# Optimization experiments

Hardware: AMD Instinct MI355X
Metric: run time of the kernel (lower is better)

The kernel has to match this reference:

```python
import jax, jax.numpy as jnp
import numpy as np

D = 512      # emb_size
H = 8        # attention heads
E = 8        # num experts
HID = 512    # expert MLP hidden (assumed StandardExpert = 2-layer MLP)
NTOK = 8192  # 8*1024 tokens
W_IMP = 0.01


def setup_inputs() -> dict:
    key = jax.random.key(0)
    ks = jax.random.split(key, 16)
    f = lambda i, shape, s=0.02: (jax.random.normal(ks[i], shape, jnp.float32) * s)
    return {
        "x": jax.random.normal(ks[0], (8, 1024, D), jnp.float32),
        "q": jax.random.normal(ks[1], (NTOK, D), jnp.float32),
        "Wq": f(2, (D, D)), "bq": jnp.zeros((D,), jnp.float32),
        "Wk": f(3, (D, D)), "bk": jnp.zeros((D,), jnp.float32),
        "Wv": f(4, (D, D)), "bv": jnp.zeros((D,), jnp.float32),
        "Wo": f(5, (D, D)), "bo": jnp.zeros((D,), jnp.float32),
        "gate_W": f(6, (D, E)), "gate_b": jnp.zeros((E,), jnp.float32),
        "W1": f(7, (E, D, HID)), "b1": jnp.zeros((E, HID), jnp.float32),
        "W2": f(8, (E, HID, D)), "b2": jnp.zeros((E, D), jnp.float32),
        "top": 2,
    }


def _cross_att(xf, q, Wq, bq, Wk, bk, Wv, bv, Wo, bo):
    # seq_len == 1 on both sides after unsqueeze(1) in the torch code
    N, d = xf.shape
    dh = d // H
    Q = (xf @ Wq + bq).reshape(N, H, dh)
    K = (q @ Wk + bk).reshape(N, H, dh)
    V = (q @ Wv + bv).reshape(N, H, dh)
    scores = jnp.sum(Q * K, axis=-1, keepdims=True) / jnp.sqrt(jnp.float32(dh))  # [N,H,1]
    w = jax.nn.softmax(scores, axis=-1)  # trivially ones (single key), kept for fidelity
    att = (w * V).reshape(N, d)
    return att @ Wo + bo


def reference(x, q, Wq, bq, Wk, bk, Wv, bv, Wo, bo, gate_W, gate_b, W1, b1, W2, b2, top):
    x_shape = x.shape
    xf = x.reshape(-1, x_shape[-1])  # [N, D]
    att = _cross_att(xf, q, Wq, bq, Wk, bk, Wv, bv, Wo, bo)
    gate_logits = att @ gate_W + gate_b
    gate_prob = jax.nn.softmax(gate_logits, axis=-1)  # [N, E] (eval mode: no noise)
    top_w, top_i = jax.lax.top_k(gate_prob, top)       # [N, top]
    top_w = jax.nn.softmax(top_w, axis=-1)
    # combine weights per expert: comb[n,e] = sum_k top_w[n,k] * [top_i[n,k]==e]
    comb = jnp.sum(top_w[..., None] * jax.nn.one_hot(top_i, E, dtype=xf.dtype), axis=1)  # [N, E]
    y = jnp.zeros_like(xf)
    for e in range(E):  # fixed small expert loop; dense compute + mask-combine
        h = jax.nn.relu(xf @ W1[e] + b1[e])
        ye = h @ W2[e] + b2[e]
        y = y + comb[:, e:e + 1] * ye
    importance = gate_prob.sum(axis=0)  # [E]
    # torch.std uses ddof=1
    importance_loss = W_IMP * (jnp.std(importance, ddof=1) / jnp.mean(importance)) ** 2
    return y.reshape(x_shape), gate_prob, importance_loss
```

## Files before the change

### kernel.cpp

```cpp
#include <hip/hip_runtime.h>
#include <math.h>
#include <stdint.h>

#define NTOK 8192
#define DIM  512
#define NEXP 8
#define HIDN 512
#define BM 64
#define BN 128
#define BK 32
#define NT  (DIM / BK)
#define MAXRB 136
#define SLOTS (MAXRB*BM)
#define GBLK (NTOK/16)

typedef _Float16 f16;
typedef __attribute__((ext_vector_type(4))) _Float16 f16x4;
typedef __attribute__((ext_vector_type(8))) _Float16 f16x8;
typedef __attribute__((ext_vector_type(4))) float    f32x4;

__device__ __forceinline__ void gl2lds16(const void* g, void* l) {
  __builtin_amdgcn_global_load_lds(
      (const __attribute__((address_space(1))) unsigned int*)(g),
      (__attribute__((address_space(3))) unsigned int*)(l), 16, 0, 0);
}

__global__ __launch_bounds__(256) void k_prep(
    const float* __restrict__ x, f16* __restrict__ xh,
    const float* __restrict__ W1, const float* __restrict__ W2,
    f16* __restrict__ W1t, f16* __restrict__ W2t,
    const float* __restrict__ Wo, const float* __restrict__ gW,
    double* __restrict__ G1) {
  const int bx = blockIdx.x, tid = threadIdx.x;
  if (bx < 4096) {
    int i4 = (bx * 256 + tid) * 4;
    float4 v = *(const float4*)(x + i4);
    f16x4 o; o.x = (_Float16)v.x; o.y = (_Float16)v.y; o.z = (_Float16)v.z; o.w = (_Float16)v.w;
    *(f16x4*)(xh + i4) = o;
  } else if (bx < 8192) {
    __shared__ float t[32][33];
    int idx = bx - 4096;
    int z = idx >> 8, rem = idx & 255;
    int k0 = (rem >> 4) * 32, n0 = (rem & 15) * 32;
    const float* src = (z < 8 ? W1 : W2) + (size_t)(z & 7) * DIM * DIM;
    f16* dst = (z < 8 ? W1t : W2t) + (size_t)(z & 7) * DIM * DIM;
    int tx = tid & 31, ty = tid >> 5;
    for (int r = ty; r < 32; r += 8) t[r][tx] = src[(size_t)(k0 + r) * DIM + n0 + tx];
    __syncthreads();
    for (int r = ty; r < 32; r += 8) dst[(size_t)(n0 + r) * DIM + k0 + tx] = (f16)t[tx][r];
  } else {
    int out = (bx - 8192) * 4 + (tid >> 6);
    int lane = tid & 63;
    int d = out >> 3, e = out & 7;
    double acc = 0.0;
#pragma unroll
    for (int j = 0; j < 8; j++) {
      int k = j * 64 + lane;
      acc += (double)Wo[d * DIM + k] * (double)gW[k * NEXP + e];
    }
#pragma unroll
    for (int off = 32; off; off >>= 1) acc += __shfl_xor(acc, off, 64);
    if (lane == 0) G1[out] = acc;
  }
}

__global__ void k_foldB(const float* __restrict__ Wv, const double* __restrict__ G1,
                        float* __restrict__ Wg, const float* __restrict__ bv,
                        const float* __restrict__ bo, const float* __restrict__ gW,
                        const float* __restrict__ gb, double* __restrict__ bg) {
  int lane = threadIdx.x & 63;
  if (blockIdx.x == 1024) {
    int w = threadIdx.x >> 6;
    for (int e = w; e < NEXP; e += 4) {
      double acc = 0.0;
#pragma unroll
      for (int j = 0; j < 8; j++) {
        int d = j * 64 + lane;
        acc += (double)bv[d] * G1[d * NEXP + e] + (double)bo[d] * (double)gW[d * NEXP + e];
      }
#pragma unroll
      for (int off = 32; off; off >>= 1) acc += __shfl_xor(acc, off, 64);
      if (lane == 0) bg[e] = acc + (double)gb[e];
    }
    return;
  }
  int out = blockIdx.x * 4 + (threadIdx.x >> 6);
  int d = out >> 3, e = out & 7;
  double acc = 0.0;
#pragma unroll
  for (int j = 0; j < 8; j++) {
    int k = j * 64 + lane;
    acc += (double)Wv[d * DIM + k] * G1[k * NEXP + e];
  }
#pragma unroll
  for (int off = 32; off; off >>= 1) acc += __shfl_xor(acc, off, 64);
  if (lane == 0) Wg[out] = (float)acc;
}

__global__ __launch_bounds__(256) void k_gate(
    const float* __restrict__ q, const float* __restrict__ Wg,
    const double* __restrict__ bg, float* __restrict__ gp_out,
    int* __restrict__ e1a, int* __restrict__ e2a,
    float* __restrict__ w1a, float* __restrict__ w2a,
    int* __restrict__ r1a, int* __restrict__ r2a, int* __restrict__ hist,
    float* __restrict__ gpsum) {
  __shared__ float qs[16 * 513];
  __shared__ float ps[16][8];
  __shared__ int cnt[16];
  const int tid = threadIdx.x;
  const int tok0 = blockIdx.x * 16;

  for (int i = tid; i < 16 * 512; i += 256) {
    int r = i >> 9, c = i & 511;
    qs[r * 513 + c] = q[(size_t)(tok0 + r) * DIM + c];
  }
  if (tid < 16) cnt[tid] = 0;
  __syncthreads();

  const int e = tid & 7;
  const int half = (tid >> 3) & 1;
  const int tl = tid >> 4;
  const float* qrow = qs + tl * 513 + half * 256;
  const float* wcol = Wg + half * 256 * NEXP + e;

  double a0 = 0, a1 = 0, a2 = 0, a3 = 0;
#pragma unroll 4
  for (int j = 0; j < 256; j += 4) {
    a0 += (double)qrow[j]     * (double)wcol[(size_t)j * NEXP];
    a1 += (double)qrow[j + 1] * (double)wcol[(size_t)(j + 1) * NEXP];
    a2 += (double)qrow[j + 2] * (double)wcol[(size_t)(j + 2) * NEXP];
    a3 += (double)qrow[j + 3] * (double)wcol[(size_t)(j + 3) * NEXP];
  }
  double acc = (a0 + a1) + (a2 + a3);
  acc += __shfl_xor(acc, 8, 64);

  double l = acc + bg[e];
  double m = l;
#pragma unroll
  for (int off = 1; off < 8; off <<= 1) m = fmax(m, __shfl_xor(m, off, 64));
  float ex = expf((float)(l - m));
  float s = ex;
#pragma unroll
  for (int off = 1; off < 8; off <<= 1) s += __shfl_xor(s, off, 64);
  float pf = ex / s;
  int tok = tok0 + tl;
  if (half == 0) { gp_out[(size_t)tok * NEXP + e] = pf; ps[tl][e] = pf; }

  double v1 = l; int i1 = e;
#pragma unroll
  for (int off = 1; off < 8; off <<= 1) {
    double ov = __shfl_xor(v1, off, 64);
    int oi = __shfl_xor(i1, off, 64);
    if (ov > v1 || (ov == v1 && oi < i1)) { v1 = ov; i1 = oi; }
  }
  double v2 = (e == i1) ? -1e300 : l; int i2 = e;
#pragma unroll
  for (int off = 1; off < 8; off <<= 1) {
    double ov = __shfl_xor(v2, off, 64);
    int oi = __shfl_xor(i2, off, 64);
    if (ov > v2 || (ov == v2 && oi < i2)) { v2 = ov; i2 = oi; }
  }
  float p1 = __shfl(pf, (tl << 4) + i1, 64);
  float p2 = __shfl(pf, (tl << 4) + i2, 64);
  if (e == 0 && half == 0) {
    float ev = expf(p2 - p1);
    float iw = 1.0f / (1.0f + ev);
    e1a[tok] = i1; e2a[tok] = i2;
    w1a[tok] = iw; w2a[tok] = ev * iw;
    r1a[tok] = atomicAdd(&cnt[i1], 1);
    r2a[tok] = atomicAdd(&cnt[8 + i2], 1);
  }
  __syncthreads();
  if (tid < 16) hist[blockIdx.x * 16 + tid] = cnt[tid];
  if (tid < 8) {
    float ssum = 0.f;
#pragma unroll
    for (int r = 0; r < 16; r++) ssum += ps[r][tid];
    gpsum[blockIdx.x * 8 + tid] = ssum;
  }
}

__global__ __launch_bounds__(1024) void k_route(
    const int* __restrict__ hist,
    const int* __restrict__ e1a, const int* __restrict__ e2a,
    const float* __restrict__ w1a, const float* __restrict__ w2a,
    const int* __restrict__ r1a, const int* __restrict__ r2a,
    int* __restrict__ aoff, int* __restrict__ counts,
    int* __restrict__ toks, float* __restrict__ wsl,
    const float* __restrict__ gpsum, float* __restrict__ loss) {
  __shared__ int bb[GBLK][16];
  __shared__ int tot[16];
  __shared__ int s_ao[16];
  __shared__ double imp[8];
  const int c = threadIdx.x >> 6;
  const int l = threadIdx.x & 63;
  int v[GBLK / 64];
  int s = 0;
#pragma unroll
  for (int j = 0; j < GBLK / 64; j++) {
    v[j] = hist[((l * (GBLK / 64) + j) << 4) + c];
    s += v[j];
  }
  int incl = s;
#pragma unroll
  for (int off = 1; off < 64; off <<= 1) {
    int t = __shfl_up(incl, off, 64);
    if (l >= off) incl += t;
  }
  int run = incl - s;
#pragma unroll
  for (int j = 0; j < GBLK / 64; j++) {
    bb[l * (GBLK / 64) + j][c] = run;
    run += v[j];
  }
  if (l == 63) tot[c] = incl;
  __syncthreads();
  if (threadIdx.x == 0) {
    int o0 = 0, o1 = 0;
#pragma unroll
    for (int e = 0; e < NEXP; e++) {
      s_ao[e] = o0;     o0 += (tot[e] + BM - 1) / BM * BM;
      s_ao[8 + e] = o1; o1 += (tot[8 + e] + BM - 1) / BM * BM;
    }
    if (blockIdx.x == 0) {
      int p0 = 0, p1 = 0;
#pragma unroll
      for (int e = 0; e < NEXP; e++) {
        counts[e] = tot[e];         aoff[e] = p0;     p0 += (tot[e] + BM - 1) / BM * BM;
        counts[8 + e] = tot[8 + e]; aoff[9 + e] = p1; p1 += (tot[8 + e] + BM - 1) / BM * BM;
      }
      aoff[8] = p0; aoff[17] = p1;
    }
  }
  __syncthreads();
  if (blockIdx.x == 0) {
    const int cnt_c = tot[c];
    const int padded = (cnt_c + BM - 1) / BM * BM;
    const int base = ((c >> 3) ? SLOTS : 0) + s_ao[c];
    for (int sidx = cnt_c + l; sidx < padded; sidx += 64)
      toks[base + sidx] = 0;
    if (c < 8) {
      double a = 0.0;
#pragma unroll
      for (int j = 0; j < GBLK / 64; j++)
        a += (double)gpsum[(size_t)(l + j * 64) * 8 + c];
#pragma unroll
      for (int off = 32; off; off >>= 1) a += __shfl_xor(a, off, 64);
      if (l == 0) imp[c] = a;
    }
    __syncthreads();
    if (threadIdx.x == 0) {
      double mn = 0.0;
      for (int e = 0; e < 8; e++) mn += imp[e];
      mn *= (1.0 / 8.0);
      double var = 0.0;
      for (int e = 0; e < 8; e++) { double d = imp[e] - mn; var += d * d; }
      var *= (1.0 / 7.0);
      double r = sqrt(var) / mn;
      loss[0] = (float)(0.01 * r * r);
    }
  }
  if (threadIdx.x < 256) {
    int n = blockIdx.x * 256 + threadIdx.x;
    int blk = n >> 4;
    int e1 = e1a[n];
    int slot = s_ao[e1] + bb[blk][e1] + r1a[n];
    toks[slot] = n; wsl[slot] = w1a[n];
    int e2 = e2a[n];
    slot = SLOTS + s_ao[8 + e2] + bb[blk][8 + e2] + r2a[n];
    toks[slot] = n; wsl[slot] = w2a[n];
  }
}

template <int MODE>
__global__ __launch_bounds__(256) void k_expert(
    const f16* __restrict__ Asrc, const f16* __restrict__ Wt,
    const float* __restrict__ bias, const int* __restrict__ toks,
    const float* __restrict__ wsl, const int* __restrict__ aoff,
    const int* __restrict__ counts, f16* __restrict__ Hout,
    float* __restrict__ y, float* __restrict__ ypart) {
  const int klist = blockIdx.z;
  const int* ao = aoff + klist * 9;
  const int slot0 = blockIdx.x * BM;
  if (slot0 >= ao[8]) return;
  int e = 0;
#pragma unroll
  for (int t = 1; t <= 7; t++) if (slot0 >= ao[t]) e = t;

  const int n0 = blockIdx.y * BN;
  const int tid = threadIdx.x, lane = tid & 63, wid = tid >> 6;

  __shared__ __align__(16) f16 As[2][BM * BK];
  __shared__ __align__(16) f16 Bs[2][BN * BK];

  const int srow = wid * 16 + (lane >> 2);
  const int scol = (lane & 3) * 8;

  const f16* arow;
  if (MODE == 0) {
    int tk = toks[klist * SLOTS + slot0 + srow];
    arow = Asrc + (size_t)tk * DIM + scol;
  } else {
    arow = Asrc + (size_t)(klist * SLOTS + slot0 + srow) * HIDN + scol;
  }
  const f16* brow[2];
  int bloff[2];
#pragma unroll
  for (int rnd = 0; rnd < 2; rnd++) {
    brow[rnd] = Wt + ((size_t)e * DIM + n0 + rnd * 64 + srow) * DIM + scol;
    bloff[rnd] = (rnd * 64 + wid * 16) * BK;
  }
  const int aloff = wid * 16 * BK;

  f32x4 acc[4][2] = {};
  const int fr = lane & 15, kb = (lane >> 4) * 8;

#define STAGE(buf, ks)                                    \
  {                                                       \
    gl2lds16(arow + (ks), As[buf] + aloff);               \
    _Pragma("unroll")                                     \
    for (int rnd = 0; rnd < 2; rnd++)                     \
      gl2lds16(brow[rnd] + (ks), Bs[buf] + bloff[rnd]);   \
  }

  STAGE(0, 0);
  __syncthreads();
  for (int t = 0; t < NT; t++) {
    const int cur = t & 1;
    if (t + 1 < NT) STAGE(cur ^ 1, (t + 1) * BK);
    f16x8 af[4], bf[2];
#pragma unroll
    for (int m = 0; m < 4; m++)
      af[m] = *(const f16x8*)(As[cur] + (m * 16 + fr) * BK + kb);
#pragma unroll
    for (int n = 0; n < 2; n++)
      bf[n] = *(const f16x8*)(Bs[cur] + (wid * 32 + n * 16 + fr) * BK + kb);
#pragma unroll
    for (int m = 0; m < 4; m++)
#pragma unroll
      for (int n = 0; n < 2; n++)
        acc[m][n] = __builtin_amdgcn_mfma_f32_16x16x32_f16(af[m], bf[n], acc[m][n], 0, 0, 0);
    __syncthreads();
  }
#undef STAGE

  float bcol[2];
#pragma unroll
  for (int n = 0; n < 2; n++)
    bcol[n] = bias[e * ((MODE == 0) ? HIDN : DIM) + n0 + wid * 32 + n * 16 + fr];

  if (MODE == 0) {
#pragma unroll
    for (int m = 0; m < 4; m++)
#pragma unroll
      for (int r4 = 0; r4 < 4; r4++) {
        int slot = slot0 + m * 16 + (lane >> 4) * 4 + r4;
#pragma unroll
        for (int n = 0; n < 2; n++) {
          int col = n0 + wid * 32 + n * 16 + fr;
          float v = acc[m][n][r4] + bcol[n];
          Hout[(size_t)(klist * SLOTS + slot) * HIDN + col] = (f16)fmaxf(v, 0.f);
        }
      }
  } else {
    float* yo = (klist == 0) ? y : ypart;
    const int vend = ao[e] + counts[klist * 8 + e];
#pragma unroll
    for (int m = 0; m < 4; m++)
#pragma unroll
      for (int r4 = 0; r4 < 4; r4++) {
        int slot = slot0 + m * 16 + (lane >> 4) * 4 + r4;
        if (slot < vend) {
          int tk = toks[klist * SLOTS + slot];
          float w = wsl[klist * SLOTS + slot];
#pragma unroll
          for (int n = 0; n < 2; n++) {
            int col = n0 + wid * 32 + n * 16 + fr;
            yo[(size_t)tk * DIM + col] = (acc[m][n][r4] + bcol[n]) * w;
          }
        }
      }
  }
}

__global__ __launch_bounds__(256) void k_combine(float* __restrict__ y,
                                                 const float* __restrict__ ypart) {
  size_t i4 = ((size_t)blockIdx.x * 256 + threadIdx.x) * 4;
  float4 a = *(const float4*)(y + i4);
  float4 b = *(const float4*)(ypart + i4);
  a.x += b.x; a.y += b.y; a.z += b.z; a.w += b.w;
  *(float4*)(y + i4) = a;
}

extern "C" void kernel_launch(void* const* d_in, const int* in_sizes, int n_in,
                              void* d_out, int out_size, void* d_ws, size_t ws_size,
                              hipStream_t stream) {
  const float* x  = (const float*)d_in[0];
  const float* q  = (const float*)d_in[1];
  const float* Wv = (const float*)d_in[6];
  const float* bv = (const float*)d_in[7];
  const float* Wo = (const float*)d_in[8];
  const float* bo = (const float*)d_in[9];
  const float* gW = (const float*)d_in[10];
  const float* gb = (const float*)d_in[11];
  const float* W1 = (const float*)d_in[12];
  const float* b1 = (const float*)d_in[13];
  const float* W2 = (const float*)d_in[14];
  const float* b2 = (const float*)d_in[15];

  float* out = (float*)d_out;
  float* y_out = out;
  float* gp_out = out + (size_t)NTOK * DIM;
  float* loss_out = gp_out + (size_t)NTOK * NEXP;

  uint8_t* w = (uint8_t*)d_ws;
  size_t o = 0;
  auto alloc = [&](size_t bytes) -> void* {
    void* p = w + o;
    o = (o + bytes + 255) & ~(size_t)255;
    return p;
  };
  f16* xh      = (f16*)alloc((size_t)NTOK * DIM * 2);
  f16* W1t     = (f16*)alloc((size_t)NEXP * DIM * HIDN * 2);
  f16* W2t     = (f16*)alloc((size_t)NEXP * DIM * HIDN * 2);
  f16* Hbuf    = (f16*)alloc((size_t)2 * SLOTS * HIDN * 2);
  float* ypart = (float*)alloc((size_t)NTOK * DIM * 4);
  double* G1   = (double*)alloc((size_t)DIM * NEXP * 8);
  float* Wg    = (float*)alloc((size_t)DIM * NEXP * 4);
  double* bg   = (double*)alloc(NEXP * 8);
  int* e1a     = (int*)alloc(NTOK * 4);
  int* e2a     = (int*)alloc(NTOK * 4);
  float* w1a   = (float*)alloc(NTOK * 4);
  float* w2a   = (float*)alloc(NTOK * 4);
  int* r1a     = (int*)alloc(NTOK * 4);
  int* r2a     = (int*)alloc(NTOK * 4);
  int* hist    = (int*)alloc((size_t)GBLK * 16 * 4);
  float* gpsum = (float*)alloc((size_t)GBLK * 8 * 4);
  int* counts  = (int*)alloc(16 * 4);
  int* aoff    = (int*)alloc(18 * 4);
  int* toks    = (int*)alloc((size_t)2 * SLOTS * 4);
  float* wsl   = (float*)alloc((size_t)2 * SLOTS * 4);
  (void)ws_size; (void)in_sizes; (void)n_in; (void)out_size;

  k_prep<<<9216, 256, 0, stream>>>(x, xh, W1, W2, W1t, W2t, Wo, gW, G1);
  k_foldB<<<1025, 256, 0, stream>>>(Wv, G1, Wg, bv, bo, gW, gb, bg);
  k_gate<<<GBLK, 256, 0, stream>>>(q, Wg, bg, gp_out, e1a, e2a, w1a, w2a, r1a, r2a, hist, gpsum);
  k_route<<<NTOK / 256, 1024, 0, stream>>>(hist, e1a, e2a, w1a, w2a, r1a, r2a,
                                           aoff, counts, toks, wsl, gpsum, loss_out);
  k_expert<0><<<dim3(MAXRB, 4, 2), 256, 0, stream>>>(xh, W1t, b1, toks, wsl, aoff, counts,
                                                     Hbuf, nullptr, nullptr);
  k_expert<1><<<dim3(MAXRB, 4, 2), 256, 0, stream>>>(Hbuf, W2t, b2, toks, wsl, aoff, counts,
                                                     nullptr, y_out, ypart);
  k_combine<<<NTOK * DIM / 1024, 256, 0, stream>>>(y_out, ypart);
}
```

Baseline: 103.0 us.

## Fuse prep, fold, gate and route into one cooperative kernel with grid syncs

Replaces four front-end launches (prep, foldB, gate, route) with a single cooperative kernel of 512 blocks that walks each phase in a grid-stride loop and separates phases with grid.sync(). The goal is to remove launch gaps and tail idle time between small dependent kernels. The routing prefix sum is now recomputed redundantly per block from the global histogram, and the work-bearing phases run on fewer resident blocks. Grid barriers add their own latency and cap parallelism at the 512 co-resident blocks.

```diff
diff --git a/kernel.cpp b/kernel.cpp
--- a/kernel.cpp
+++ b/kernel.cpp
@@ -1,6 +1,9 @@
 #include <hip/hip_runtime.h>
+#include <hip/hip_cooperative_groups.h>
 #include <math.h>
 #include <stdint.h>
+
+namespace cg = cooperative_groups;
 
 #define NTOK 8192
 #define DIM  512
@@ -13,6 +16,7 @@
 #define MAXRB 136
 #define SLOTS (MAXRB*BM)
 #define GBLK (NTOK/16)
+#define FBLK 512
 
 typedef _Float16 f16;
 typedef __attribute__((ext_vector_type(4))) _Float16 f16x4;
@@ -25,250 +29,252 @@
       (__attribute__((address_space(3))) unsigned int*)(l), 16, 0, 0);
 }
 
-__global__ __launch_bounds__(256) void k_prep(
-    const float* __restrict__ x, f16* __restrict__ xh,
-    const float* __restrict__ W1, const float* __restrict__ W2,
-    f16* __restrict__ W1t, f16* __restrict__ W2t,
-    const float* __restrict__ Wo, const float* __restrict__ gW,
-    double* __restrict__ G1) {
-  const int bx = blockIdx.x, tid = threadIdx.x;
-  if (bx < 4096) {
-    int i4 = (bx * 256 + tid) * 4;
-    float4 v = *(const float4*)(x + i4);
-    f16x4 o; o.x = (_Float16)v.x; o.y = (_Float16)v.y; o.z = (_Float16)v.z; o.w = (_Float16)v.w;
-    *(f16x4*)(xh + i4) = o;
-  } else if (bx < 8192) {
-    __shared__ float t[32][33];
-    int idx = bx - 4096;
-    int z = idx >> 8, rem = idx & 255;
-    int k0 = (rem >> 4) * 32, n0 = (rem & 15) * 32;
-    const float* src = (z < 8 ? W1 : W2) + (size_t)(z & 7) * DIM * DIM;
-    f16* dst = (z < 8 ? W1t : W2t) + (size_t)(z & 7) * DIM * DIM;
-    int tx = tid & 31, ty = tid >> 5;
-    for (int r = ty; r < 32; r += 8) t[r][tx] = src[(size_t)(k0 + r) * DIM + n0 + tx];
-    __syncthreads();
-    for (int r = ty; r < 32; r += 8) dst[(size_t)(n0 + r) * DIM + k0 + tx] = (f16)t[tx][r];
-  } else {
-    int out = (bx - 8192) * 4 + (tid >> 6);
+struct FrontArgs {
+  const float* x;  f16* xh;
+  const float* W1; const float* W2; f16* W1t; f16* W2t;
+  const float* Wo; const float* gW; double* G1;
+  const float* Wv; const float* bv; const float* bo; const float* gb;
+  float* Wg; double* bg;
+  const float* q;  float* gp_out;
+  int* e1a; int* e2a; float* w1a; float* w2a; int* r1a; int* r2a;
+  int* hist; float* gpsum;
+  int* aoff; int* counts; int* toks; float* wsl; float* loss;
+};
+
+union SMem {
+  struct { float qs[16 * 513]; float ps[16][8]; int cnt[16]; } g;
+  struct { float t[32][33]; } tr;
+  struct {
+    int sfull[16][16]; int sbelow[16][16];
+    int tot[16]; int pre[16]; int s_ao[16];
+    double simp[32][8]; double imp[8];
+  } r;
+};
+
+__global__ __launch_bounds__(256) void k_front(FrontArgs a) {
+  cg::grid_group grid = cg::this_grid();
+  __shared__ SMem sm;
+  const int tid = threadIdx.x;
+  const int b = blockIdx.x;
+
+  for (int u = b; u < 9216; u += FBLK) {
+    if (u < 4096) {
+      int i4 = (u * 256 + tid) * 4;
+      float4 v = *(const float4*)(a.x + i4);
+      f16x4 o; o.x = (_Float16)v.x; o.y = (_Float16)v.y; o.z = (_Float16)v.z; o.w = (_Float16)v.w;
+      *(f16x4*)(a.xh + i4) = o;
+    } else if (u < 8192) {
+      int idx = u - 4096;
+      int z = idx >> 8, rem = idx & 255;
+      int k0 = (rem >> 4) * 32, n0 = (rem & 15) * 32;
+      const float* src = (z < 8 ? a.W1 : a.W2) + (size_t)(z & 7) * DIM * DIM;
+      f16* dst = (z < 8 ? a.W1t : a.W2t) + (size_t)(z & 7) * DIM * DIM;
+      int tx = tid & 31, ty = tid >> 5;
+      __syncthreads();
+      for (int r = ty; r < 32; r += 8) sm.tr.t[r][tx] = src[(size_t)(k0 + r) * DIM + n0 + tx];
+      __syncthreads();
+      for (int r = ty; r < 32; r += 8) dst[(size_t)(n0 + r) * DIM + k0 + tx] = (f16)sm.tr.t[tx][r];
+      __syncthreads();
+    } else {
+      int out = (u - 8192) * 4 + (tid >> 6);
+      int lane = tid & 63;
+      int d = out >> 3, e = out & 7;
+      double acc = 0.0;
+#pragma unroll
+      for (int j = 0; j < 8; j++) {
+        int k = j * 64 + lane;
+        acc += (double)a.Wo[d * DIM + k] * (double)a.gW[k * NEXP + e];
+      }
+#pragma unroll
+      for (int off = 32; off; off >>= 1) acc += __shfl_xor(acc, off, 64);
+      if (lane == 0) a.G1[out] = acc;
+    }
+  }
+  grid.sync();
+
+  for (int u = b; u < 1025; u += FBLK) {
     int lane = tid & 63;
-    int d = out >> 3, e = out & 7;
-    double acc = 0.0;
-#pragma unroll
-    for (int j = 0; j < 8; j++) {
-      int k = j * 64 + lane;
-      acc += (double)Wo[d * DIM + k] * (double)gW[k * NEXP + e];
-    }
-#pragma unroll
-    for (int off = 32; off; off >>= 1) acc += __shfl_xor(acc, off, 64);
-    if (lane == 0) G1[out] = acc;
-  }
-}
-
-__global__ void k_foldB(const float* __restrict__ Wv, const double* __restrict__ G1,
-                        float* __restrict__ Wg, const float* __restrict__ bv,
-                        const float* __restrict__ bo, const float* __restrict__ gW,
-                        const float* __restrict__ gb, double* __restrict__ bg) {
-  int lane = threadIdx.x & 63;
-  if (blockIdx.x == 1024) {
-    int w = threadIdx.x >> 6;
-    for (int e = w; e < NEXP; e += 4) {
+    if (u == 1024) {
+      int w = tid >> 6;
+      for (int e = w; e < NEXP; e += 4) {
+        double acc = 0.0;
+#pragma unroll
+        for (int j = 0; j < 8; j++) {
+          int d = j * 64 + lane;
+          acc += (double)a.bv[d] * a.G1[d * NEXP + e] + (double)a.bo[d] * (double)a.gW[d * NEXP + e];
+        }
+#pragma unroll
+        for (int off = 32; off; off >>= 1) acc += __shfl_xor(acc, off, 64);
+        if (lane == 0) a.bg[e] = acc + (double)a.gb[e];
+      }
+    } else {
+      int out = u * 4 + (tid >> 6);
+      int d = out >> 3, e = out & 7;
       double acc = 0.0;
 #pragma unroll
       for (int j = 0; j < 8; j++) {
-        int d = j * 64 + lane;
-        acc += (double)bv[d] * G1[d * NEXP + e] + (double)bo[d] * (double)gW[d * NEXP + e];
+        int k = j * 64 + lane;
+        acc += (double)a.Wv[d * DIM + k] * a.G1[k * NEXP + e];
       }
 #pragma unroll
       for (int off = 32; off; off >>= 1) acc += __shfl_xor(acc, off, 64);
-      if (lane == 0) bg[e] = acc + (double)gb[e];
-    }
-    return;
-  }
-  int out = blockIdx.x * 4 + (threadIdx.x >> 6);
-  int d = out >> 3, e = out & 7;
-  double acc = 0.0;
-#pragma unroll
-  for (int j = 0; j < 8; j++) {
-    int k = j * 64 + lane;
-    acc += (double)Wv[d * DIM + k] * G1[k * NEXP + e];
-  }
-#pragma unroll
-  for (int off = 32; off; off >>= 1) acc += __shfl_xor(acc, off, 64);
-  if (lane == 0) Wg[out] = (float)acc;
-}
-
-__global__ __launch_bounds__(256) void k_gate(
-    const float* __restrict__ q, const float* __restrict__ Wg,
-    const double* __restrict__ bg, float* __restrict__ gp_out,
-    int* __restrict__ e1a, int* __restrict__ e2a,
-    float* __restrict__ w1a, float* __restrict__ w2a,
-    int* __restrict__ r1a, int* __restrict__ r2a, int* __restrict__ hist,
-    float* __restrict__ gpsum) {
-  __shared__ float qs[16 * 513];
-  __shared__ float ps[16][8];
-  __shared__ int cnt[16];
-  const int tid = threadIdx.x;
-  const int tok0 = blockIdx.x * 16;
-
-  for (int i = tid; i < 16 * 512; i += 256) {
-    int r = i >> 9, c = i & 511;
-    qs[r * 513 + c] = q[(size_t)(tok0 + r) * DIM + c];
-  }
-  if (tid < 16) cnt[tid] = 0;
-  __syncthreads();
-
-  const int e = tid & 7;
-  const int half = (tid >> 3) & 1;
-  const int tl = tid >> 4;
-  const float* qrow = qs + tl * 513 + half * 256;
-  const float* wcol = Wg + half * 256 * NEXP + e;
-
-  double a0 = 0, a1 = 0, a2 = 0, a3 = 0;
+      if (lane == 0) a.Wg[out] = (float)acc;
+    }
+  }
+  grid.sync();
+
+  {
+    const int tok0 = b * 16;
+    __syncthreads();
+    for (int i = tid; i < 16 * 512; i += 256) {
+      int r = i >> 9, c = i & 511;
+      sm.g.qs[r * 513 + c] = a.q[(size_t)(tok0 + r) * DIM + c];
+    }
+    if (tid < 16) sm.g.cnt[tid] = 0;
+    __syncthreads();
+
+    const int e = tid & 7;
+    const int half = (tid >> 3) & 1;
+    const int tl = tid >> 4;
+    const float* qrow = sm.g.qs + tl * 513 + half * 256;
+    const float* wcol = a.Wg + half * 256 * NEXP + e;
+
+    double a0 = 0, a1 = 0, a2 = 0, a3 = 0;
 #pragma unroll 4
-  for (int j = 0; j < 256; j += 4) {
-    a0 += (double)qrow[j]     * (double)wcol[(size_t)j * NEXP];
-    a1 += (double)qrow[j + 1] * (double)wcol[(size_t)(j + 1) * NEXP];
-    a2 += (double)qrow[j + 2] * (double)wcol[(size_t)(j + 2) * NEXP];
-    a3 += (double)qrow[j + 3] * (double)wcol[(size_t)(j + 3) * NEXP];
-  }
-  double acc = (a0 + a1) + (a2 + a3);
-  acc += __shfl_xor(acc, 8, 64);
-
-  double l = acc + bg[e];
-  double m = l;
-#pragma unroll
-  for (int off = 1; off < 8; off <<= 1) m = fmax(m, __shfl_xor(m, off, 64));
-  float ex = expf((float)(l - m));
-  float s = ex;
-#pragma unroll
-  for (int off = 1; off < 8; off <<= 1) s += __shfl_xor(s, off, 64);
-  float pf = ex / s;
-  int tok = tok0 + tl;
-  if (half == 0) { gp_out[(size_t)tok * NEXP + e] = pf; ps[tl][e] = pf; }
-
-  double v1 = l; int i1 = e;
-#pragma unroll
-  for (int off = 1; off < 8; off <<= 1) {
-    double ov = __shfl_xor(v1, off, 64);
-    int oi = __shfl_xor(i1, off, 64);
-    if (ov > v1 || (ov == v1 && oi < i1)) { v1 = ov; i1 = oi; }
-  }
-  double v2 = (e == i1) ? -1e300 : l; int i2 = e;
-#pragma unroll
-  for (int off = 1; off < 8; off <<= 1) {
-    double ov = __shfl_xor(v2, off, 64);
-    int oi = __shfl_xor(i2, off, 64);
-    if (ov > v2 || (ov == v2 && oi < i2)) { v2 = ov; i2 = oi; }
-  }
-  float p1 = __shfl(pf, (tl << 4) + i1, 64);
-  float p2 = __shfl(pf, (tl << 4) + i2, 64);
-  if (e == 0 && half == 0) {
-    float ev = expf(p2 - p1);
-    float iw = 1.0f / (1.0f + ev);
-    e1a[tok] = i1; e2a[tok] = i2;
-    w1a[tok] = iw; w2a[tok] = ev * iw;
-    r1a[tok] = atomicAdd(&cnt[i1], 1);
-    r2a[tok] = atomicAdd(&cnt[8 + i2], 1);
-  }
-  __syncthreads();
-  if (tid < 16) hist[blockIdx.x * 16 + tid] = cnt[tid];
-  if (tid < 8) {
-    float ssum = 0.f;
-#pragma unroll
-    for (int r = 0; r < 16; r++) ssum += ps[r][tid];
-    gpsum[blockIdx.x * 8 + tid] = ssum;
-  }
-}
-
-__global__ __launch_bounds__(1024) void k_route(
-    const int* __restrict__ hist,
-    const int* __restrict__ e1a, const int* __restrict__ e2a,
-    const float* __restrict__ w1a, const float* __restrict__ w2a,
-    const int* __restrict__ r1a, const int* __restrict__ r2a,
-    int* __restrict__ aoff, int* __restrict__ counts,
-    int* __restrict__ toks, float* __restrict__ wsl,
-    const float* __restrict__ gpsum, float* __restrict__ loss) {
-  __shared__ int bb[GBLK][16];
-  __shared__ int tot[16];
-  __shared__ int s_ao[16];
-  __shared__ double imp[8];
-  const int c = threadIdx.x >> 6;
-  const int l = threadIdx.x & 63;
-  int v[GBLK / 64];
-  int s = 0;
-#pragma unroll
-  for (int j = 0; j < GBLK / 64; j++) {
-    v[j] = hist[((l * (GBLK / 64) + j) << 4) + c];
-    s += v[j];
-  }
-  int incl = s;
-#pragma unroll
-  for (int off = 1; off < 64; off <<= 1) {
-    int t = __shfl_up(incl, off, 64);
-    if (l >= off) incl += t;
-  }
-  int run = incl - s;
-#pragma unroll
-  for (int j = 0; j < GBLK / 64; j++) {
-    bb[l * (GBLK / 64) + j][c] = run;
-    run += v[j];
-  }
-  if (l == 63) tot[c] = incl;
-  __syncthreads();
-  if (threadIdx.x == 0) {
-    int o0 = 0, o1 = 0;
-#pragma unroll
-    for (int e = 0; e < NEXP; e++) {
-      s_ao[e] = o0;     o0 += (tot[e] + BM - 1) / BM * BM;
-      s_ao[8 + e] = o1; o1 += (tot[8 + e] + BM - 1) / BM * BM;
-    }
-    if (blockIdx.x == 0) {
-      int p0 = 0, p1 = 0;
+    for (int j = 0; j < 256; j += 4) {
+      a0 += (double)qrow[j]     * (double)wcol[(size_t)j * NEXP];
+      a1 += (double)qrow[j + 1] * (double)wcol[(size_t)(j + 1) * NEXP];
+      a2 += (double)qrow[j + 2] * (double)wcol[(size_t)(j + 2) * NEXP];
+      a3 += (double)qrow[j + 3] * (double)wcol[(size_t)(j + 3) * NEXP];
+    }
+    double acc = (a0 + a1) + (a2 + a3);
+    acc += __shfl_xor(acc, 8, 64);
+
+    double l = acc + a.bg[e];
+    double m = l;
+#pragma unroll
+    for (int off = 1; off < 8; off <<= 1) m = fmax(m, __shfl_xor(m, off, 64));
+    float ex = expf((float)(l - m));
+    float s = ex;
+#pragma unroll
+    for (int off = 1; off < 8; off <<= 1) s += __shfl_xor(s, off, 64);
+    float pf = ex / s;
+    int tok = tok0 + tl;
+    if (half == 0) { a.gp_out[(size_t)tok * NEXP + e] = pf; sm.g.ps[tl][e] = pf; }
+
+    double v1 = l; int i1 = e;
+#pragma unroll
+    for (int off = 1; off < 8; off <<= 1) {
+      double ov = __shfl_xor(v1, off, 64);
+      int oi = __shfl_xor(i1, off, 64);
+      if (ov > v1 || (ov == v1 && oi < i1)) { v1 = ov; i1 = oi; }
+    }
+    double v2 = (e == i1) ? -1e300 : l; int i2 = e;
+#pragma unroll
+    for (int off = 1; off < 8; off <<= 1) {
+      double ov = __shfl_xor(v2, off, 64);
+      int oi = __shfl_xor(i2, off, 64);
+      if (ov > v2 || (ov == v2 && oi < i2)) { v2 = ov; i2 = oi; }
+    }
+    float p1 = __shfl(pf, (tl << 4) + i1, 64);
+    float p2 = __shfl(pf, (tl << 4) + i2, 64);
+    if (e == 0 && half == 0) {
+      float ev = expf(p2 - p1);
+      float iw = 1.0f / (1.0f + ev);
+      a.e1a[tok] = i1; a.e2a[tok] = i2;
+      a.w1a[tok] = iw; a.w2a[tok] = ev * iw;
+      a.r1a[tok] = atomicAdd(&sm.g.cnt[i1], 1);
+      a.r2a[tok] = atomicAdd(&sm.g.cnt[8 + i2], 1);
+    }
+    __syncthreads();
+    if (tid < 16) a.hist[b * 16 + tid] = sm.g.cnt[tid];
+    if (tid < 8) {
+      float ssum = 0.f;
+#pragma unroll
+      for (int r = 0; r < 16; r++) ssum += sm.g.ps[r][tid];
+      a.gpsum[b * 8 + tid] = ssum;
+    }
+  }
+  grid.sync();
+
+  {
+    const int c = tid & 15, seg = tid >> 4;
+    int fullsum = 0, belowsum = 0;
+    for (int j = 0; j < 32; j++) {
+      int blk = seg * 32 + j;
+      int h = a.hist[blk * 16 + c];
+      fullsum += h;
+      if (blk < b) belowsum += h;
+    }
+    __syncthreads();
+    sm.r.sfull[seg][c] = fullsum; sm.r.sbelow[seg][c] = belowsum;
+    __syncthreads();
+    if (tid < 16) {
+      int f = 0, bl = 0;
+#pragma unroll
+      for (int s2 = 0; s2 < 16; s2++) { f += sm.r.sfull[s2][tid]; bl += sm.r.sbelow[s2][tid]; }
+      sm.r.tot[tid] = f; sm.r.pre[tid] = bl;
+    }
+    __syncthreads();
+    if (tid == 0) {
+      int o0 = 0, o1 = 0;
 #pragma unroll
       for (int e = 0; e < NEXP; e++) {
-        counts[e] = tot[e];         aoff[e] = p0;     p0 += (tot[e] + BM - 1) / BM * BM;
-        counts[8 + e] = tot[8 + e]; aoff[9 + e] = p1; p1 += (tot[8 + e] + BM - 1) / BM * BM;
-      }
-      aoff[8] = p0; aoff[17] = p1;
-    }
-  }
-  __syncthreads();
-  if (blockIdx.x == 0) {
-    const int cnt_c = tot[c];
-    const int padded = (cnt_c + BM - 1) / BM * BM;
-    const int base = ((c >> 3) ? SLOTS : 0) + s_ao[c];
-    for (int sidx = cnt_c + l; sidx < padded; sidx += 64)
-      toks[base + sidx] = 0;
-    if (c < 8) {
-      double a = 0.0;
-#pragma unroll
-      for (int j = 0; j < GBLK / 64; j++)
-        a += (double)gpsum[(size_t)(l + j * 64) * 8 + c];
-#pragma unroll
-      for (int off = 32; off; off >>= 1) a += __shfl_xor(a, off, 64);
-      if (l == 0) imp[c] = a;
-    }
-    __syncthreads();
-    if (threadIdx.x == 0) {
-      double mn = 0.0;
-      for (int e = 0; e < 8; e++) mn += imp[e];
-      mn *= (1.0 / 8.0);
-      double var = 0.0;
-      for (int e = 0; e < 8; e++) { double d = imp[e] - mn; var += d * d; }
-      var *= (1.0 / 7.0);
-      double r = sqrt(var) / mn;
-      loss[0] = (float)(0.01 * r * r);
-    }
-  }
-  if (threadIdx.x < 256) {
-    int n = blockIdx.x * 256 + threadIdx.x;
-    int blk = n >> 4;
-    int e1 = e1a[n];
-    int slot = s_ao[e1] + bb[blk][e1] + r1a[n];
-    toks[slot] = n; wsl[slot] = w1a[n];
-    int e2 = e2a[n];
-    slot = SLOTS + s_ao[8 + e2] + bb[blk][8 + e2] + r2a[n];
-    toks[slot] = n; wsl[slot] = w2a[n];
+        sm.r.s_ao[e] = o0;     o0 += (sm.r.tot[e] + BM - 1) / BM * BM;
+        sm.r.s_ao[8 + e] = o1; o1 += (sm.r.tot[8 + e] + BM - 1) / BM * BM;
+      }
+      if (b == 0) {
+        int p0 = 0, p1 = 0;
+#pragma unroll
+        for (int e = 0; e < NEXP; e++) {
+          a.counts[e] = sm.r.tot[e];         a.aoff[e] = p0;     p0 += (sm.r.tot[e] + BM - 1) / BM * BM;
+          a.counts[8 + e] = sm.r.tot[8 + e]; a.aoff[9 + e] = p1; p1 += (sm.r.tot[8 + e] + BM - 1) / BM * BM;
+        }
+        a.aoff[8] = p0; a.aoff[17] = p1;
+      }
+    }
+    __syncthreads();
+    if (b == 0) {
+      const int cc = tid >> 4, ll = tid & 15;
+      const int cnt_c = sm.r.tot[cc];
+      const int padded = (cnt_c + BM - 1) / BM * BM;
+      const int base = ((cc >> 3) ? SLOTS : 0) + sm.r.s_ao[cc];
+      for (int sidx = cnt_c + ll; sidx < padded; sidx += 16)
+        a.toks[base + sidx] = 0;
+      {
+        const int e = tid & 7, j0 = tid >> 3;
+        double acc2 = 0.0;
+        for (int k = 0; k < 16; k++)
+          acc2 += (double)a.gpsum[(size_t)(j0 + 32 * k) * 8 + e];
+        sm.r.simp[j0][e] = acc2;
+      }
+      __syncthreads();
+      if (tid < 8) {
+        double s2 = 0.0;
+        for (int j = 0; j < 32; j++) s2 += sm.r.simp[j][tid];
+        sm.r.imp[tid] = s2;
+      }
+      __syncthreads();
+      if (tid == 0) {
+        double mn = 0.0;
+        for (int e = 0; e < 8; e++) mn += sm.r.imp[e];
+        mn *= (1.0 / 8.0);
+        double var = 0.0;
+        for (int e = 0; e < 8; e++) { double d = sm.r.imp[e] - mn; var += d * d; }
+        var *= (1.0 / 7.0);
+        double r = sqrt(var) / mn;
+        a.loss[0] = (float)(0.01 * r * r);
+      }
+    }
+    if (tid < 16) {
+      int n = b * 16 + tid;
+      int E1 = a.e1a[n];
+      int slot = sm.r.s_ao[E1] + sm.r.pre[E1] + a.r1a[n];
+      a.toks[slot] = n; a.wsl[slot] = a.w1a[n];
+      int E2 = a.e2a[n];
+      slot = SLOTS + sm.r.s_ao[8 + E2] + sm.r.pre[8 + E2] + a.r2a[n];
+      a.toks[slot] = n; a.wsl[slot] = a.w2a[n];
+    }
   }
 }
 
@@ -442,11 +448,20 @@
   float* wsl   = (float*)alloc((size_t)2 * SLOTS * 4);
   (void)ws_size; (void)in_sizes; (void)n_in; (void)out_size;
 
-  k_prep<<<9216, 256, 0, stream>>>(x, xh, W1, W2, W1t, W2t, Wo, gW, G1);
-  k_foldB<<<1025, 256, 0, stream>>>(Wv, G1, Wg, bv, bo, gW, gb, bg);
-  k_gate<<<GBLK, 256, 0, stream>>>(q, Wg, bg, gp_out, e1a, e2a, w1a, w2a, r1a, r2a, hist, gpsum);
-  k_route<<<NTOK / 256, 1024, 0, stream>>>(hist, e1a, e2a, w1a, w2a, r1a, r2a,
-                                           aoff, counts, toks, wsl, gpsum, loss_out);
+  FrontArgs fa;
+  fa.x = x; fa.xh = xh;
+  fa.W1 = W1; fa.W2 = W2; fa.W1t = W1t; fa.W2t = W2t;
+  fa.Wo = Wo; fa.gW = gW; fa.G1 = G1;
+  fa.Wv = Wv; fa.bv = bv; fa.bo = bo; fa.gb = gb;
+  fa.Wg = Wg; fa.bg = bg;
+  fa.q = q; fa.gp_out = gp_out;
+  fa.e1a = e1a; fa.e2a = e2a; fa.w1a = w1a; fa.w2a = w2a; fa.r1a = r1a; fa.r2a = r2a;
+  fa.hist = hist; fa.gpsum = gpsum;
+  fa.aoff = aoff; fa.counts = counts; fa.toks = toks; fa.wsl = wsl; fa.loss = loss_out;
+
+  void* kargs[] = { &fa };
+  hipLaunchCooperativeKernel((const void*)k_front, dim3(FBLK), dim3(256), kargs, 0, stream);
+
   k_expert<0><<<dim3(MAXRB, 4, 2), 256, 0, stream>>>(xh, W1t, b1, toks, wsl, aoff, counts,
                                                      Hbuf, nullptr, nullptr);
   k_expert<1><<<dim3(MAXRB, 4, 2), 256, 0, stream>>>(Hbuf, W2t, b2, toks, wsl, aoff, counts,
```

Result: slower. 274.8 us (+167.0%).
